# Kernel optimization log

Hardware: AMD Instinct MI355X
Metric: run time of the kernel (lower is better)

Reference implementation:

```python
import jax, jax.numpy as jnp
import numpy as np

MAXGRAD = 2.0
B, H, W, C = 8, 512, 512, 16


def _integral_image(x):
    # x: [B,H,W,2]; cumsum x-channel along width, y-channel along height
    x_s = jnp.cumsum(x[..., 0], axis=2)
    y_s = jnp.cumsum(x[..., 1], axis=1)
    return jnp.stack([x_s, y_s], axis=-1) - 1.0


def _normalize(grid):
    # grid: [B,H,W,2] -> rescale each row/col extent to [0, W-1] x [0, H-1]
    Hh, Ww = grid.shape[1], grid.shape[2]
    max_x = grid[:, :, -1:, 0]  # [B,H,1]
    min_x = grid[:, :, :1, 0]
    max_y = grid[:, -1:, :, 1]  # [B,1,W]
    min_y = grid[:, :1, :, 1]
    norm_x = (grid[..., 0] - min_x) / (max_x - min_x)
    norm_y = (grid[..., 1] - min_y) / (max_y - min_y)
    return jnp.stack([(Ww - 1) * norm_x, (Hh - 1) * norm_y], axis=-1)


def _resample2d(im, grid):
    # im: [B,H,W,C], grid: [B,H,W,2] in pixel coords; bilinear with border clamp
    Bb, Hh, Ww, _ = im.shape
    x = grid[..., 0]
    y = grid[..., 1]
    x0 = jnp.floor(x).astype(jnp.int32)
    x1 = x0 + 1
    y0 = jnp.floor(y).astype(jnp.int32)
    y1 = y0 + 1
    x0 = jnp.clip(x0, 0, Ww - 1)
    x1 = jnp.clip(x1, 0, Ww - 1)
    y0 = jnp.clip(y0, 0, Hh - 1)
    y1 = jnp.clip(y1, 0, Hh - 1)
    b = jnp.arange(Bb)[:, None, None]
    Ia = im[b, y0, x0]  # [B,H,W,C]
    Ib = im[b, y1, x0]
    Ic = im[b, y0, x1]
    Id = im[b, y1, x1]
    x0f = x0.astype(x.dtype)
    x1f = x1.astype(x.dtype)
    y0f = y0.astype(y.dtype)
    y1f = y1.astype(y.dtype)
    wa = ((x1f - x) * (y1f - y))[..., None]
    wb = ((x1f - x) * (y - y0f))[..., None]
    wc = ((x - x0f) * (y1f - y))[..., None]
    wd = ((x - x0f) * (y - y0f))[..., None]
    return wa * Ia + wb * Ib + wc * Ic + wd * Id


def setup_inputs() -> dict:
    key = jax.random.key(0)
    k1, k2, k3 = jax.random.split(key, 3)
    mov = jax.random.normal(k1, (B, H, W, C), dtype=jnp.float32)
    ref = jax.random.normal(k2, (B, H, W, C), dtype=jnp.float32)
    defgrad = jax.random.normal(k3, (B, H, W, 2), dtype=jnp.float32) * 0.1
    return {"mov": mov, "ref": ref, "defgrad": defgrad}


def reference(mov, ref, defgrad):
    c = MAXGRAD
    dg = c / (1.0 + (c - 1.0) * jnp.exp(-defgrad))  # logistic growth
    base_grid = _integral_image(jnp.ones_like(dg))
    sampling_grid = _integral_image(dg)
    grid_norm = _normalize(sampling_grid)
    grid_inv = 2.0 * base_grid - grid_norm
    mov_def = _resample2d(mov, grid_norm)
    ref_def = _resample2d(mov_def, grid_inv)
    return (mov_def, ref_def, grid_norm, grid_inv)
```

## Files before the change

kernel.cpp:

```cpp
#include <hip/hip_runtime.h>

#define Bn 8
#define Hn 512
#define Wn 512
#define Cn 16

__global__ void grid_x_kernel(const float* __restrict__ defgrad,
                              float* __restrict__ grid_norm,
                              float* __restrict__ grid_inv) {
    __shared__ float s[512];
    const int row = blockIdx.x;
    const int t   = threadIdx.x;
    const long base = (long)row * Wn;
    float g = defgrad[(base + t) * 2 + 0];
    float v = 2.0f / (1.0f + expf(-g));
    s[t] = v;
    __syncthreads();
    for (int off = 1; off < 512; off <<= 1) {
        float add = (t >= off) ? s[t - off] : 0.0f;
        __syncthreads();
        s[t] += add;
        __syncthreads();
    }
    float s0    = s[0];
    float denom = s[511] - s0;
    float norm  = 511.0f * ((s[t] - s0) / denom);
    long o = (base + t) * 2;
    grid_norm[o] = norm;
    grid_inv[o]  = 2.0f * (float)t - norm;
}

__global__ void grid_y_kernel(const float* __restrict__ defgrad,
                              float* __restrict__ grid_norm,
                              float* __restrict__ grid_inv) {
    __shared__ float partial[8][64];
    __shared__ float e0s[64];
    const int b    = blockIdx.x >> 3;
    const int w0   = (blockIdx.x & 7) * 64;
    const int wave = threadIdx.x >> 6;
    const int lane = threadIdx.x & 63;
    const int w    = w0 + lane;
    const long cbase = ((long)b * Hn) * Wn + w;

    float sum = 0.f;
    for (int i = 0; i < 64; ++i) {
        int h = wave * 64 + i;
        float g = defgrad[(cbase + (long)h * Wn) * 2 + 1];
        float v = 2.0f / (1.0f + expf(-g));
        if (wave == 0 && i == 0) e0s[lane] = v;
        sum += v;
    }
    partial[wave][lane] = sum;
    __syncthreads();

    float off = 0.f, tot = 0.f;
    for (int j = 0; j < 8; ++j) {
        float p = partial[j][lane];
        if (j < wave) off += p;
        tot += p;
    }
    float e0    = e0s[lane];
    float denom = tot - e0;

    float run = off;
    for (int i = 0; i < 64; ++i) {
        int h = wave * 64 + i;
        long pidx = cbase + (long)h * Wn;
        float g = defgrad[pidx * 2 + 1];
        float v = 2.0f / (1.0f + expf(-g));
        run += v;
        float norm = 511.0f * ((run - e0) / denom);
        grid_norm[pidx * 2 + 1] = norm;
        grid_inv[pidx * 2 + 1]  = 2.0f * (float)h - norm;
    }
}

__global__ void resample_kernel(const float* __restrict__ im,
                                const float* __restrict__ grid,
                                float* __restrict__ out) {
    long gid = (long)blockIdx.x * blockDim.x + threadIdx.x;
    long pix = gid >> 2;
    int  cg  = (int)(gid & 3);
    int  bi  = (int)(pix >> 18);

    float x = grid[pix * 2 + 0];
    float y = grid[pix * 2 + 1];
    int x0 = (int)floorf(x);
    int y0 = (int)floorf(y);
    int x1 = x0 + 1, y1 = y0 + 1;
    x0 = min(max(x0, 0), Wn - 1);
    x1 = min(max(x1, 0), Wn - 1);
    y0 = min(max(y0, 0), Hn - 1);
    y1 = min(max(y1, 0), Hn - 1);
    float x0f = (float)x0, x1f = (float)x1, y0f = (float)y0, y1f = (float)y1;
    float wa = (x1f - x) * (y1f - y);
    float wb = (x1f - x) * (y - y0f);
    float wc = (x - x0f) * (y1f - y);
    float wd = (x - x0f) * (y - y0f);

    long ib = (long)bi * ((long)Hn * Wn * Cn);
    int  co = cg * 4;
    const float4 a4 = *(const float4*)&im[ib + ((long)y0 * Wn + x0) * Cn + co];
    const float4 b4 = *(const float4*)&im[ib + ((long)y1 * Wn + x0) * Cn + co];
    const float4 c4 = *(const float4*)&im[ib + ((long)y0 * Wn + x1) * Cn + co];
    const float4 d4 = *(const float4*)&im[ib + ((long)y1 * Wn + x1) * Cn + co];

    float4 r;
    r.x = wa * a4.x + wb * b4.x + wc * c4.x + wd * d4.x;
    r.y = wa * a4.y + wb * b4.y + wc * c4.y + wd * d4.y;
    r.z = wa * a4.z + wb * b4.z + wc * c4.z + wd * d4.z;
    r.w = wa * a4.w + wb * b4.w + wc * c4.w + wd * d4.w;
    *(float4*)&out[pix * Cn + co] = r;
}

extern "C" void kernel_launch(void* const* d_in, const int* in_sizes, int n_in,
                              void* d_out, int out_size, void* d_ws, size_t ws_size,
                              hipStream_t stream) {
    const float* mov     = (const float*)d_in[0];
    const float* defgrad = (const float*)d_in[2];
    float* out = (float*)d_out;

    const long N_img  = (long)Bn * Hn * Wn * Cn;
    const long N_grid = (long)Bn * Hn * Wn * 2;
    float* mov_def   = out;
    float* ref_def   = out + N_img;
    float* grid_norm = out + 2 * N_img;
    float* grid_inv  = out + 2 * N_img + N_grid;

    grid_x_kernel<<<dim3(Bn * Hn), dim3(512), 0, stream>>>(defgrad, grid_norm, grid_inv);
    grid_y_kernel<<<dim3(Bn * (Wn / 64)), dim3(512), 0, stream>>>(defgrad, grid_norm, grid_inv);

    const long total_threads = (long)Bn * Hn * Wn * 4;
    resample_kernel<<<dim3((unsigned)(total_threads / 256)), dim3(256), 0, stream>>>(mov, grid_norm, mov_def);
    resample_kernel<<<dim3((unsigned)(total_threads / 256)), dim3(256), 0, stream>>>(mov_def, grid_inv, ref_def);
}
```

Before: 517.6 us.

## Fuse grid kernels, use wave-shuffle scan, one thread per pixel resample

Merges the x- and y-direction grid kernels into a single launch: the first 64 blocks handle column scans and the rest handle row scans, with the row scan now built from wave shuffles instead of a shared-memory Hillis-Steele scan. The resample kernel now has one thread per pixel that loads all 16 channels as four float4 vectors, and it writes output with nontemporal stores. This aims to cut launch count, scan barriers and redundant grid loads. The trade-off is fewer threads in the resample kernel, each with more outstanding loads. The change also switches to the fast __expf and pins the last normalized value to exactly 511.

```diff
diff --git a/kernel.cpp b/kernel.cpp
--- a/kernel.cpp
+++ b/kernel.cpp
@@ -5,86 +5,91 @@
 #define Wn 512
 #define Cn 16
 
-__global__ void grid_x_kernel(const float* __restrict__ defgrad,
-                              float* __restrict__ grid_norm,
-                              float* __restrict__ grid_inv) {
-    __shared__ float s[512];
-    const int row = blockIdx.x;
-    const int t   = threadIdx.x;
-    const long base = (long)row * Wn;
-    float g = defgrad[(base + t) * 2 + 0];
-    float v = 2.0f / (1.0f + expf(-g));
-    s[t] = v;
-    __syncthreads();
-    for (int off = 1; off < 512; off <<= 1) {
-        float add = (t >= off) ? s[t - off] : 0.0f;
-        __syncthreads();
-        s[t] += add;
-        __syncthreads();
-    }
-    float s0    = s[0];
-    float denom = s[511] - s0;
-    float norm  = 511.0f * ((s[t] - s0) / denom);
-    long o = (base + t) * 2;
-    grid_norm[o] = norm;
-    grid_inv[o]  = 2.0f * (float)t - norm;
-}
+typedef float fx4 __attribute__((ext_vector_type(4)));
 
-__global__ void grid_y_kernel(const float* __restrict__ defgrad,
-                              float* __restrict__ grid_norm,
-                              float* __restrict__ grid_inv) {
-    __shared__ float partial[8][64];
-    __shared__ float e0s[64];
-    const int b    = blockIdx.x >> 3;
-    const int w0   = (blockIdx.x & 7) * 64;
+__device__ __forceinline__ float dgf(float g) { return 2.0f / (1.0f + __expf(-g)); }
+
+__global__ __launch_bounds__(512) void grid_kernel(const float* __restrict__ defgrad,
+                                                   float* __restrict__ grid_norm,
+                                                   float* __restrict__ grid_inv) {
     const int wave = threadIdx.x >> 6;
     const int lane = threadIdx.x & 63;
-    const int w    = w0 + lane;
-    const long cbase = ((long)b * Hn) * Wn + w;
 
-    float sum = 0.f;
-    for (int i = 0; i < 64; ++i) {
-        int h = wave * 64 + i;
-        float g = defgrad[(cbase + (long)h * Wn) * 2 + 1];
-        float v = 2.0f / (1.0f + expf(-g));
-        if (wave == 0 && i == 0) e0s[lane] = v;
-        sum += v;
-    }
-    partial[wave][lane] = sum;
-    __syncthreads();
+    if (blockIdx.x < 64) {
+        __shared__ float partial[8][64];
+        const int b  = blockIdx.x >> 3;
+        const int w0 = (blockIdx.x & 7) * 64;
+        const int w  = w0 + lane;
+        const long cbase = ((long)b * Hn) * Wn + w;
 
-    float off = 0.f, tot = 0.f;
-    for (int j = 0; j < 8; ++j) {
-        float p = partial[j][lane];
-        if (j < wave) off += p;
-        tot += p;
-    }
-    float e0    = e0s[lane];
-    float denom = tot - e0;
+        float e0 = dgf(defgrad[cbase * 2 + 1]);
+        float sum = 0.f;
+        #pragma unroll 8
+        for (int i = 0; i < 64; ++i) {
+            int h = (wave << 6) + i;
+            sum += dgf(defgrad[(cbase + (long)h * Wn) * 2 + 1]);
+        }
+        partial[wave][lane] = sum;
+        __syncthreads();
+        float off = 0.f, tot = 0.f;
+        #pragma unroll
+        for (int j = 0; j < 8; ++j) {
+            float p = partial[j][lane];
+            if (j < wave) off += p;
+            tot += p;
+        }
+        float denom = tot - e0;
+        float run = off;
+        #pragma unroll 8
+        for (int i = 0; i < 64; ++i) {
+            int h = (wave << 6) + i;
+            long pidx = cbase + (long)h * Wn;
+            run += dgf(defgrad[pidx * 2 + 1]);
+            float norm = (h == Hn - 1) ? 511.0f : 511.0f * ((run - e0) / denom);
+            grid_norm[pidx * 2 + 1] = norm;
+            grid_inv[pidx * 2 + 1]  = 2.0f * (float)h - norm;
+        }
+    } else {
+        __shared__ float wsum[8];
+        __shared__ float s0sh;
+        const int row = blockIdx.x - 64;
+        const int t   = threadIdx.x;
+        const long base = (long)row * Wn;
 
-    float run = off;
-    for (int i = 0; i < 64; ++i) {
-        int h = wave * 64 + i;
-        long pidx = cbase + (long)h * Wn;
-        float g = defgrad[pidx * 2 + 1];
-        float v = 2.0f / (1.0f + expf(-g));
-        run += v;
-        float norm = 511.0f * ((run - e0) / denom);
-        grid_norm[pidx * 2 + 1] = norm;
-        grid_inv[pidx * 2 + 1]  = 2.0f * (float)h - norm;
+        float v = dgf(defgrad[(base + t) * 2]);
+        float x = v;
+        #pragma unroll
+        for (int o = 1; o < 64; o <<= 1) {
+            float n = __shfl_up(x, o, 64);
+            x += (lane >= o) ? n : 0.0f;
+        }
+        if (lane == 63) wsum[wave] = x;
+        if (t == 0)     s0sh = v;
+        __syncthreads();
+        float pre = 0.f, tot = 0.f;
+        #pragma unroll
+        for (int j = 0; j < 8; ++j) {
+            float p = wsum[j];
+            if (j < wave) pre += p;
+            tot += p;
+        }
+        float scan = x + pre;
+        float s0   = s0sh;
+        float norm = (t == Wn - 1) ? 511.0f : 511.0f * ((scan - s0) / (tot - s0));
+        long o = (base + t) * 2;
+        grid_norm[o] = norm;
+        grid_inv[o]  = 2.0f * (float)t - norm;
     }
 }
 
-__global__ void resample_kernel(const float* __restrict__ im,
-                                const float* __restrict__ grid,
-                                float* __restrict__ out) {
-    long gid = (long)blockIdx.x * blockDim.x + threadIdx.x;
-    long pix = gid >> 2;
-    int  cg  = (int)(gid & 3);
-    int  bi  = (int)(pix >> 18);
+__global__ __launch_bounds__(256) void resample_kernel(const float* __restrict__ im,
+                                                       const float* __restrict__ grid,
+                                                       float* __restrict__ out) {
+    const int pix = blockIdx.x * 256 + threadIdx.x;
+    const int bi  = pix >> 18;
 
-    float x = grid[pix * 2 + 0];
-    float y = grid[pix * 2 + 1];
+    float2 g = *(const float2*)&grid[(long)pix * 2];
+    float x = g.x, y = g.y;
     int x0 = (int)floorf(x);
     int y0 = (int)floorf(y);
     int x1 = x0 + 1, y1 = y0 + 1;
@@ -98,19 +103,19 @@
     float wc = (x - x0f) * (y1f - y);
     float wd = (x - x0f) * (y - y0f);
 
-    long ib = (long)bi * ((long)Hn * Wn * Cn);
-    int  co = cg * 4;
-    const float4 a4 = *(const float4*)&im[ib + ((long)y0 * Wn + x0) * Cn + co];
-    const float4 b4 = *(const float4*)&im[ib + ((long)y1 * Wn + x0) * Cn + co];
-    const float4 c4 = *(const float4*)&im[ib + ((long)y0 * Wn + x1) * Cn + co];
-    const float4 d4 = *(const float4*)&im[ib + ((long)y1 * Wn + x1) * Cn + co];
+    const float* base = im + ((long)bi << 22);
+    const fx4* A = (const fx4*)(base + (((long)(y0 << 9) + x0) << 4));
+    const fx4* Bp= (const fx4*)(base + (((long)(y1 << 9) + x0) << 4));
+    const fx4* Cp= (const fx4*)(base + (((long)(y0 << 9) + x1) << 4));
+    const fx4* Dp= (const fx4*)(base + (((long)(y1 << 9) + x1) << 4));
+    fx4* O = (fx4*)(out + ((long)pix << 4));
 
-    float4 r;
-    r.x = wa * a4.x + wb * b4.x + wc * c4.x + wd * d4.x;
-    r.y = wa * a4.y + wb * b4.y + wc * c4.y + wd * d4.y;
-    r.z = wa * a4.z + wb * b4.z + wc * c4.z + wd * d4.z;
-    r.w = wa * a4.w + wb * b4.w + wc * c4.w + wd * d4.w;
-    *(float4*)&out[pix * Cn + co] = r;
+    #pragma unroll
+    for (int c = 0; c < 4; ++c) {
+        fx4 a = A[c], b = Bp[c], cc = Cp[c], d = Dp[c];
+        fx4 r = wa * a + wb * b + wc * cc + wd * d;
+        __builtin_nontemporal_store(r, &O[c]);
+    }
 }
 
 extern "C" void kernel_launch(void* const* d_in, const int* in_sizes, int n_in,
@@ -127,10 +132,9 @@
     float* grid_norm = out + 2 * N_img;
     float* grid_inv  = out + 2 * N_img + N_grid;
 
-    grid_x_kernel<<<dim3(Bn * Hn), dim3(512), 0, stream>>>(defgrad, grid_norm, grid_inv);
-    grid_y_kernel<<<dim3(Bn * (Wn / 64)), dim3(512), 0, stream>>>(defgrad, grid_norm, grid_inv);
+    grid_kernel<<<dim3(64 + Bn * Hn), dim3(512), 0, stream>>>(defgrad, grid_norm, grid_inv);
 
-    const long total_threads = (long)Bn * Hn * Wn * 4;
-    resample_kernel<<<dim3((unsigned)(total_threads / 256)), dim3(256), 0, stream>>>(mov, grid_norm, mov_def);
-    resample_kernel<<<dim3((unsigned)(total_threads / 256)), dim3(256), 0, stream>>>(mov_def, grid_inv, ref_def);
+    const int npix = Bn * Hn * Wn;
+    resample_kernel<<<dim3(npix / 256), dim3(256), 0, stream>>>(mov, grid_norm, mov_def);
+    resample_kernel<<<dim3(npix / 256), dim3(256), 0, stream>>>(mov_def, grid_inv, ref_def);
 }
```

After: 618.5 us. 19.5% more time.
